# Kernel tuning notes

Measured on AMD Instinct MI355X. Metric: run time of the kernel, lower is better.

Reference implementation:

```python
import jax, jax.numpy as jnp
import numpy as np

THRESH = 0.5          # boundary_threshold
N_TARGET = 6.0        # target_avg_token_length
RATIO_W = 0.03        # ratio_loss_weight
LRD = 0.75            # learning_rate_difference
EPS = 1e-8            # torch cosine_similarity eps


def _frac_grad(t, frac):
    # value = t, gradient scaled by frac (straight-through)
    tg = t * frac
    return tg + jax.lax.stop_gradient(t - tg)


def _assoc_scan(gates, x):
    # h_t = gates_t * h_{t-1} + x_t, over axis 1. gates: [B,N], x: [B,N,D]
    def combine(a, b):
        ga, xa = a
        gb, xb = b
        return gb * ga, gb * xa + xb
    _, h = jax.lax.associative_scan(combine, (gates[..., None], x), axis=1)
    return h


def _forward(tokens, W_qk, start_key, W_res, b_res):
    B, L, D = tokens.shape
    # queries / keys projection
    qk = jnp.einsum('bld,de->ble', tokens, W_qk)
    q, k = jnp.split(qk, 2, axis=-1)
    # keys shifted right by one, start_key token prepended
    ks = jnp.concatenate([jnp.broadcast_to(start_key, (B, 1, k.shape[-1])), k[:, :-1]], axis=1)
    qn = jnp.linalg.norm(q, axis=-1)
    kn = jnp.linalg.norm(ks, axis=-1)
    cos = jnp.sum(q * ks, axis=-1) / jnp.maximum(qn * kn, EPS)
    probs = (1.0 - cos) * 0.5                              # [B,L]
    boundary = (probs > THRESH).at[:, 0].set(True)         # [B,L] bool
    num_chunks = boundary.sum(-1)                          # [B]
    chunk_id = jnp.cumsum(boundary.astype(jnp.int32), axis=1) - 1  # token -> chunk slot
    b_idx = jnp.broadcast_to(jnp.arange(B)[:, None], (B, L))
    slot = jnp.where(boundary, chunk_id, L)                # pad slot L for non-boundaries
    # padded (to worst-case L chunks) boundary tokens / probs — equals nested_tensor.to_padded_tensor
    down = jnp.zeros((B, L + 1, D), tokens.dtype).at[b_idx, slot].set(tokens)[:, :L]
    bprobs = jnp.zeros((B, L + 1), probs.dtype).at[b_idx, slot].set(probs)[:, :L]
    chunk_lens = jnp.zeros((B, L), jnp.int32).at[b_idx, chunk_id].add(1)  # tokens per chunk, 0-padded
    mask = jnp.arange(L)[None, :] < num_chunks[:, None]    # valid chunk slots
    gates = 1.0 - bprobs
    down = down * bprobs[..., None]
    confidence = jnp.where(boundary, probs, 1.0 - probs)
    scale = confidence + jax.lax.stop_gradient(1.0 - confidence)  # straight_through(confidence, 1.0)
    # aux ratio loss (straight-through fraction vectors)
    F_soft = jax.nn.sigmoid(probs - THRESH)
    F = (F_soft + jax.lax.stop_gradient(boundary.astype(probs.dtype) - F_soft)).mean(-1)
    G = probs.mean(-1)
    aux = (N_TARGET / (N_TARGET - 1.0)) * ((N_TARGET - 1.0) * F * G + (1.0 - F) * (1.0 - G))
    weighted_aux = aux.mean() * RATIO_W
    downsampled = _frac_grad(down, 1.0 / LRD)
    # ---- upsample(downsampled) ----
    scanned = _assoc_scan(gates, downsampled)              # smooth assoc scan over chunk slots
    # repeat_interleave by chunk_lens == gather chunk vector for each token position
    ups = jnp.take_along_axis(scanned, chunk_id[..., None], axis=1)  # [B,L,D]
    ups = ups * scale[..., None]
    ups = ups + jnp.einsum('bld,de->ble', tokens, W_res) + b_res     # residual_proj(residual)
    ups = _frac_grad(ups, LRD)
    return downsampled, ups, weighted_aux


def setup_inputs() -> dict:
    key = jax.random.key(0)
    k1, k2, k3, k4 = jax.random.split(key, 4)
    B, L, D, DQK = 8, 4096, 1024, 1024
    return {
        'tokens': jax.random.normal(k1, (B, L, D), jnp.float32),
        'W_qk': jax.random.normal(k2, (D, 2 * DQK), jnp.float32) * 0.02,
        'start_key': jax.random.normal(k3, (DQK,), jnp.float32) * 0.01,
        'W_res': jax.random.normal(k4, (D, D), jnp.float32) * 0.02,
        'b_res': jnp.zeros((D,), jnp.float32),
    }


def reference(tokens, W_qk, start_key, W_res, b_res):
    return _forward(tokens, W_qk, start_key, W_res, b_res)
```

## Files before the change

### kernel.cpp

```cpp
#include <hip/hip_runtime.h>
#include <hip/hip_fp16.h>
#include <cmath>

typedef unsigned short u16;
typedef _Float16 halfT;
typedef halfT v8h __attribute__((ext_vector_type(8)));
typedef float v4f __attribute__((ext_vector_type(4)));

#define B_   8
#define L_   4096
#define D_   1024
#define M_   32768
#define RCAP 8192

__global__ __launch_bounds__(256) void split_tok(const float* __restrict__ T,
    u16* __restrict__ Tf) {
  size_t id = (size_t)blockIdx.x * 256 + threadIdx.x;
  size_t base = id * 8;
  float4 v0 = *(const float4*)(T + base);
  float4 v1 = *(const float4*)(T + base + 4);
  float a[8] = {v0.x, v0.y, v0.z, v0.w, v1.x, v1.y, v1.z, v1.w};
  u16 h[8];
#pragma unroll
  for (int j = 0; j < 8; j++) h[j] = __half_as_ushort(__float2half(a[j]));
  *(uint4*)(Tf + base) = *(uint4*)h;
}

__global__ __launch_bounds__(256) void split_wT(const float* __restrict__ W,
    int N, u16* __restrict__ Wf) {
  int id = blockIdx.x * 256 + threadIdx.x;
  int n = id & (N - 1);
  int k0 = (id / N) * 8;
  u16 h[8];
#pragma unroll
  for (int j = 0; j < 8; j++)
    h[j] = __half_as_ushort(__float2half(W[(size_t)(k0 + j) * N + n]));
  *(uint4*)(Wf + (size_t)n * 1024 + k0) = *(uint4*)h;
}

__device__ __forceinline__ void gll16(const void* g, void* l) {
  __builtin_amdgcn_global_load_lds(
      (const __attribute__((address_space(1))) void*)g,
      (__attribute__((address_space(3))) void*)l, 16, 0, 0);
}

__global__ __launch_bounds__(256) void gemm_f16(
    const u16* __restrict__ Af, const u16* __restrict__ Bf,
    void* __restrict__ Cout, int N, int NTN, int mode,
    const float* __restrict__ Hs, const int* __restrict__ cid,
    const float* __restrict__ bres)
{
  __shared__ u16 ldsA[4096], ldsB[4096];
  const int tid = threadIdx.x;
  const int lane = tid & 63, w = tid >> 6;
  const int q = lane >> 4, fr = lane & 15;
  const int wr = w >> 1, wc = w & 1;
  int bid = blockIdx.x;
  int idx = bid >> 3, x = bid & 7;
  const int n0 = (idx % NTN) * 128;
  const int m0 = (x * 32 + idx / NTN) * 128;

  const u16* src = (w < 2) ? Af : Bf;
  const int rowbase = ((w < 2) ? m0 : n0) + (w & 1) * 64;
  u16* dst = ((w < 2) ? ldsA : ldsB) + (w & 1) * 2048;

  v4f acc[4][4];
#pragma unroll
  for (int i = 0; i < 4; i++)
#pragma unroll
    for (int j = 0; j < 4; j++) acc[i][j] = (v4f)0.f;

  for (int kt = 0; kt < 32; kt++) {
    const u16* sk = src + kt * 32;
#pragma unroll
    for (int j = 0; j < 4; j++) {
      int lam = j * 64 + lane;
      int mi = lam >> 2;
      int qq = (lam & 3) ^ ((lam >> 3) & 3);
      gll16(sk + (size_t)(rowbase + mi) * 1024 + qq * 8, dst + j * 512);
    }
    __syncthreads();
    v8h bh[4];
#pragma unroll
    for (int nt = 0; nt < 4; nt++) {
      int r = wc * 64 + nt * 16 + fr;
      int off = r * 32 + ((q ^ ((r >> 1) & 3)) << 3);
      bh[nt] = *(const v8h*)&ldsB[off];
    }
#pragma unroll
    for (int mt = 0; mt < 4; mt++) {
      int r = wr * 64 + mt * 16 + fr;
      int off = r * 32 + ((q ^ ((r >> 1) & 3)) << 3);
      v8h ah = *(const v8h*)&ldsA[off];
#pragma unroll
      for (int nt = 0; nt < 4; nt++)
        acc[mt][nt] = __builtin_amdgcn_mfma_f32_16x16x32_f16(ah, bh[nt], acc[mt][nt], 0, 0, 0);
    }
    __syncthreads();
  }

  if (mode == 0) {
    __half* C = (__half*)Cout;
#pragma unroll
    for (int mt = 0; mt < 4; mt++)
#pragma unroll
      for (int r = 0; r < 4; r++) {
        int grow = m0 + wr * 64 + mt * 16 + q * 4 + r;
        __half* crow = C + (size_t)grow * N + n0 + wc * 64 + fr;
#pragma unroll
        for (int nt = 0; nt < 4; nt++)
          crow[nt * 16] = __float2half(acc[mt][nt][r]);
      }
  } else {
    float* C = (float*)Cout;
#pragma unroll
    for (int mt = 0; mt < 4; mt++)
#pragma unroll
      for (int r = 0; r < 4; r++) {
        int grow = m0 + wr * 64 + mt * 16 + q * 4 + r;
        int b = grow >> 12;
        int cc = cid[grow];
        const float* hrow = Hs + (size_t)((b << 12) + cc) * 1024 + n0 + wc * 64 + fr;
        const float* brow = bres + n0 + wc * 64 + fr;
        float* crow = C + (size_t)grow * 1024 + n0 + wc * 64 + fr;
#pragma unroll
        for (int nt = 0; nt < 4; nt++)
          crow[nt * 16] = acc[mt][nt][r] + hrow[nt * 16] + brow[nt * 16];
      }
  }
}

__global__ __launch_bounds__(256) void probs_half(const __half* __restrict__ C1,
    const float* __restrict__ skey, float* __restrict__ probs)
{
  int gt = blockIdx.x * 256 + threadIdx.x;
  int wid = gt >> 6, lane = threadIdx.x & 63;
  float qv[16], kv[16];
  {
    const __half2* p2 = (const __half2*)(C1 + (size_t)wid * 2048 + lane * 16);
#pragma unroll
    for (int j = 0; j < 8; j++) {
      float2 f = __half22float2(p2[j]); qv[2 * j] = f.x; qv[2 * j + 1] = f.y;
    }
  }
  if ((wid & 4095) == 0) {
#pragma unroll
    for (int j = 0; j < 16; j++) kv[j] = skey[lane * 16 + j];
  } else {
    const __half2* p2 = (const __half2*)(C1 + (size_t)(wid - 1) * 2048 + 1024 + lane * 16);
#pragma unroll
    for (int j = 0; j < 8; j++) {
      float2 f = __half22float2(p2[j]); kv[2 * j] = f.x; kv[2 * j + 1] = f.y;
    }
  }
  float dq = 0.f, nq = 0.f, nk = 0.f;
#pragma unroll
  for (int j = 0; j < 16; j++) {
    dq += qv[j] * kv[j]; nq += qv[j] * qv[j]; nk += kv[j] * kv[j];
  }
#pragma unroll
  for (int off = 32; off > 0; off >>= 1) {
    dq += __shfl_down(dq, off);
    nq += __shfl_down(nq, off);
    nk += __shfl_down(nk, off);
  }
  if (lane == 0)
    probs[wid] = 0.5f * (1.f - dq / fmaxf(sqrtf(nq) * sqrtf(nk), 1e-8f));
}

__global__ void zero_cnt(int* __restrict__ cnt) {
  if (threadIdx.x == 0) *cnt = 0;
}

__global__ __launch_bounds__(256) void flag_kernel(
    const float* __restrict__ probs, int* __restrict__ flags,
    int* __restrict__ cnt)
{
  int gm = blockIdx.x * 256 + threadIdx.x;
  float cosv = 1.f - 2.f * probs[gm];
  if (fabsf(cosv) < 2.5e-4f) {
    int idx = atomicAdd(cnt, 1);
    if (idx < RCAP) flags[idx] = gm;
  }
}

__global__ __launch_bounds__(256) void recheck2(
    const float* __restrict__ tok, const float* __restrict__ Wqk,
    const float* __restrict__ sk, float* __restrict__ probs,
    const int* __restrict__ flags, const int* __restrict__ cnt)
{
  __shared__ float sq[1024], sp[1024];
  __shared__ double red[3][4];
  int nf = *cnt; if (nf > RCAP) nf = RCAP;
  int t = threadIdx.x;
  for (int fi = blockIdx.x; fi < nf; fi += gridDim.x) {
    int gm = flags[fi];
    int l = gm & 4095;
    const float* trow = tok + (size_t)gm * 1024;
    for (int j = t; j < 1024; j += 256) {
      sq[j] = trow[j];
      sp[j] = l ? trow[j - 1024] : 0.f;
    }
    __syncthreads();
    double qe0 = 0, qe1 = 0, qe2 = 0, qe3 = 0;
    double ke0 = 0, ke1 = 0, ke2 = 0, ke3 = 0;
    const float4* wq = (const float4*)Wqk + t;
    const float4* wk = (const float4*)(Wqk + 1024) + t;
#pragma unroll 4
    for (int d = 0; d < 1024; d++) {
      double td = (double)sq[d];
      double pd = (double)sp[d];
      float4 a = wq[(size_t)d * 512];
      float4 b = wk[(size_t)d * 512];
      qe0 += td * (double)a.x; qe1 += td * (double)a.y;
      qe2 += td * (double)a.z; qe3 += td * (double)a.w;
      ke0 += pd * (double)b.x; ke1 += pd * (double)b.y;
      ke2 += pd * (double)b.z; ke3 += pd * (double)b.w;
    }
    if (l == 0) {
      float4 s4 = *((const float4*)sk + t);
      ke0 = (double)s4.x; ke1 = (double)s4.y;
      ke2 = (double)s4.z; ke3 = (double)s4.w;
    }
    double dq = qe0 * ke0 + qe1 * ke1 + qe2 * ke2 + qe3 * ke3;
    double nq = qe0 * qe0 + qe1 * qe1 + qe2 * qe2 + qe3 * qe3;
    double nk = ke0 * ke0 + ke1 * ke1 + ke2 * ke2 + ke3 * ke3;
#pragma unroll
    for (int off = 32; off > 0; off >>= 1) {
      dq += __shfl_down(dq, off);
      nq += __shfl_down(nq, off);
      nk += __shfl_down(nk, off);
    }
    int w = t >> 6;
    if ((t & 63) == 0) { red[0][w] = dq; red[1][w] = nq; red[2][w] = nk; }
    __syncthreads();
    if (t == 0) {
      double DQ = red[0][0] + red[0][1] + red[0][2] + red[0][3];
      double NQ = red[1][0] + red[1][1] + red[1][2] + red[1][3];
      double NK = red[2][0] + red[2][1] + red[2][2] + red[2][3];
      double den = sqrt(NQ) * sqrt(NK);
      if (den < 1e-8) den = 1e-8;
      probs[gm] = (float)(0.5 * (1.0 - DQ / den));
    }
    __syncthreads();
  }
}

__global__ __launch_bounds__(256) void meta_kernel(
    const float* __restrict__ probs, int* __restrict__ cid,
    int* __restrict__ pos, float* __restrict__ cprob,
    int* __restrict__ numC, float* __restrict__ auxv)
{
  __shared__ int   sc[256];
  __shared__ float psh[256];
  int b = blockIdx.x, t = threadIdx.x;
  const float* pr = probs + b * 4096;
  int base = t * 16;
  float pv[16]; int loc[16]; bool bd[16];
  int cnt = 0; float ps = 0.f;
#pragma unroll
  for (int i = 0; i < 16; i++) {
    float p = pr[base + i];
    pv[i] = p; ps += p;
    bool bb = (base + i == 0) || (p > 0.5f);
    bd[i] = bb; cnt += bb ? 1 : 0; loc[i] = cnt;
  }
  sc[t] = cnt; psh[t] = ps;
  __syncthreads();
  for (int off = 1; off < 256; off <<= 1) {
    int add = (t >= off) ? sc[t - off] : 0;
    __syncthreads();
    sc[t] += add;
    __syncthreads();
  }
  int excl = sc[t] - cnt;
#pragma unroll
  for (int i = 0; i < 16; i++) {
    int c = excl + loc[i] - 1;
    cid[b * 4096 + base + i] = c;
    if (bd[i]) { pos[b * 4096 + c] = base + i; cprob[b * 4096 + c] = pv[i]; }
  }
  int total = sc[255];
  for (int off = 128; off > 0; off >>= 1) {
    if (t < off) psh[t] += psh[t + off];
    __syncthreads();
  }
  if (t == 0) {
    numC[b] = total;
    float F = (float)total / 4096.f;
    float G = psh[0] / 4096.f;
    auxv[b] = 1.2f * (5.f * F * G + (1.f - F) * (1.f - G));
  }
}

__global__ void aux_final(const float* __restrict__ auxv, float* __restrict__ out2)
{
  if (threadIdx.x == 0) {
    float s = 0.f;
    for (int i = 0; i < 8; i++) s += auxv[i];
    out2[0] = s * (0.03f / 8.f);
  }
}

__global__ __launch_bounds__(256) void down_kernel(
    const float* __restrict__ tok, const int* __restrict__ pos,
    const float* __restrict__ cprob, const int* __restrict__ numC,
    float* __restrict__ out0)
{
  int blk = blockIdx.x;
  int b = blk >> 12, slot = blk & 4095;
  float4 v = make_float4(0.f, 0.f, 0.f, 0.f);
  if (slot < numC[b]) {
    int l = pos[blk];
    float p = cprob[blk];
    float4 tv = *(const float4*)(tok + (size_t)((b << 12) + l) * 1024 + threadIdx.x * 4);
    v = make_float4(p * tv.x, p * tv.y, p * tv.z, p * tv.w);
  }
  *(float4*)(out0 + (size_t)blk * 1024 + threadIdx.x * 4) = v;
}

__global__ __launch_bounds__(256) void scanH_kernel(
    const float* __restrict__ out0, const float* __restrict__ cprob,
    const int* __restrict__ numC, float* __restrict__ H)
{
  int seg = blockIdx.x, b = blockIdx.y;
  int nc = numC[b];
  int cs = seg << 8;
  if (cs >= nc) return;
  int ce = min(cs + 256, nc);
  int c0 = (seg == 0) ? 0 : cs - 64;
  int off = threadIdx.x * 4;
  float hx = 0.f, hy = 0.f, hz = 0.f, hw = 0.f;
  int c = c0;
  for (; c < cs; c++) {
    float g = 1.f - cprob[(b << 12) + c];
    float4 xv = *(const float4*)(out0 + (size_t)((b << 12) + c) * 1024 + off);
    hx = fmaf(g, hx, xv.x); hy = fmaf(g, hy, xv.y);
    hz = fmaf(g, hz, xv.z); hw = fmaf(g, hw, xv.w);
  }
  for (; c < ce; c++) {
    float g = 1.f - cprob[(b << 12) + c];
    float4 xv = *(const float4*)(out0 + (size_t)((b << 12) + c) * 1024 + off);
    hx = fmaf(g, hx, xv.x); hy = fmaf(g, hy, xv.y);
    hz = fmaf(g, hz, xv.z); hw = fmaf(g, hw, xv.w);
    *(float4*)(H + (size_t)((b << 12) + c) * 1024 + off) = make_float4(hx, hy, hz, hw);
  }
}

extern "C" void kernel_launch(void* const* d_in, const int* in_sizes, int n_in,
                              void* d_out, int out_size, void* d_ws, size_t ws_size,
                              hipStream_t stream)
{
  const float* tokens = (const float*)d_in[0];
  const float* Wqk    = (const float*)d_in[1];
  const float* sk     = (const float*)d_in[2];
  const float* Wres   = (const float*)d_in[3];
  const float* bres   = (const float*)d_in[4];

  float* out0 = (float*)d_out;
  float* out1 = out0 + (size_t)M_ * D_;
  float* out2 = out1 + (size_t)M_ * D_;

  char* ws = (char*)d_ws;
  __half* C1h  = (__half*)ws;
  float*  Hbuf = (float*)ws;
  int*   rflags = (int*)ws;
  int*   rcnt   = (int*)(ws + (size_t)RCAP * 4);
  u16* Tf = (u16*)(ws + 134217728ull);
  u16* Wf = (u16*)(ws + 268435456ull);
  float* probs = (float*)(ws + 276824064ull);
  int*   cidp  = (int*)(ws + 276955136ull);
  int*   posp  = (int*)(ws + 277086208ull);
  float* cprob = (float*)(ws + 277217280ull);
  int*   numC  = (int*)(ws + 277348352ull);
  float* auxv  = (float*)(ws + 277348416ull);

  split_tok<<<16384, 256, 0, stream>>>(tokens, Tf);
  split_wT<<<1024, 256, 0, stream>>>(Wqk, 2048, Wf);
  gemm_f16<<<4096, 256, 0, stream>>>(Tf, Wf, C1h, 2048, 16, 0,
                                     nullptr, nullptr, nullptr);
  probs_half<<<8192, 256, 0, stream>>>(C1h, sk, probs);
  zero_cnt<<<1, 64, 0, stream>>>(rcnt);
  flag_kernel<<<128, 256, 0, stream>>>(probs, rflags, rcnt);
  recheck2<<<512, 256, 0, stream>>>(tokens, Wqk, sk, probs, rflags, rcnt);
  meta_kernel<<<8, 256, 0, stream>>>(probs, cidp, posp, cprob, numC, auxv);
  aux_final<<<1, 64, 0, stream>>>(auxv, out2);
  down_kernel<<<M_, 256, 0, stream>>>(tokens, posp, cprob, numC, out0);
  scanH_kernel<<<dim3(16, 8), 256, 0, stream>>>(out0, cprob, numC, Hbuf);
  split_wT<<<512, 256, 0, stream>>>(Wres, 1024, Wf);
  gemm_f16<<<2048, 256, 0, stream>>>(Tf, Wf, out1, 1024, 8, 1,
                                     Hbuf, cidp, bres);
}
```

Baseline: 992.1 us.

## Double GEMM K-tile, fuse flagging into probs kernel, vectorize half loads

The GEMM now stages a K=64 slice per iteration instead of K=32, using 8-wide XOR swizzling. This halves the loop iterations and barrier pairs, at the cost of twice the LDS footprint per block. The separate flag kernel is folded into probs_half, which now flags near-zero cosines with an atomic, and its half loads are widened to uint4. Recheck flags move into the out1 buffer, and the Wres transpose is hoisted into its own buffer early, removing one launch and reordering the small kernels.

```diff
diff --git a/kernel.cpp b/kernel.cpp
--- a/kernel.cpp
+++ b/kernel.cpp
@@ -50,7 +50,7 @@
     const float* __restrict__ Hs, const int* __restrict__ cid,
     const float* __restrict__ bres)
 {
-  __shared__ u16 ldsA[4096], ldsB[4096];
+  __shared__ u16 ldsA[8192], ldsB[8192];
   const int tid = threadIdx.x;
   const int lane = tid & 63, w = tid >> 6;
   const int q = lane >> 4, fr = lane & 15;
@@ -62,7 +62,10 @@
 
   const u16* src = (w < 2) ? Af : Bf;
   const int rowbase = ((w < 2) ? m0 : n0) + (w & 1) * 64;
-  u16* dst = ((w < 2) ? ldsA : ldsB) + (w & 1) * 2048;
+  u16* dst = ((w < 2) ? ldsA : ldsB) + (w & 1) * 4096;
+
+  const int lhi = lane >> 3;
+  const int swz = (lane & 7) ^ lhi;
 
   v4f acc[4][4];
 #pragma unroll
@@ -70,31 +73,34 @@
 #pragma unroll
     for (int j = 0; j < 4; j++) acc[i][j] = (v4f)0.f;
 
-  for (int kt = 0; kt < 32; kt++) {
-    const u16* sk = src + kt * 32;
-#pragma unroll
-    for (int j = 0; j < 4; j++) {
-      int lam = j * 64 + lane;
-      int mi = lam >> 2;
-      int qq = (lam & 3) ^ ((lam >> 3) & 3);
-      gll16(sk + (size_t)(rowbase + mi) * 1024 + qq * 8, dst + j * 512);
-    }
-    __syncthreads();
-    v8h bh[4];
+  for (int kt = 0; kt < 16; kt++) {
+    const u16* sk = src + kt * 64;
+#pragma unroll
+    for (int j = 0; j < 8; j++) {
+      int mi = j * 8 + lhi;
+      gll16(sk + (size_t)(rowbase + mi) * 1024 + swz * 8, dst + j * 512);
+    }
+    __syncthreads();
+    v8h bh[4][2];
 #pragma unroll
     for (int nt = 0; nt < 4; nt++) {
       int r = wc * 64 + nt * 16 + fr;
-      int off = r * 32 + ((q ^ ((r >> 1) & 3)) << 3);
-      bh[nt] = *(const v8h*)&ldsB[off];
+#pragma unroll
+      for (int kk = 0; kk < 2; kk++) {
+        int off = r * 64 + (((q + 4 * kk) ^ (r & 7)) << 3);
+        bh[nt][kk] = *(const v8h*)&ldsB[off];
+      }
     }
 #pragma unroll
     for (int mt = 0; mt < 4; mt++) {
       int r = wr * 64 + mt * 16 + fr;
-      int off = r * 32 + ((q ^ ((r >> 1) & 3)) << 3);
-      v8h ah = *(const v8h*)&ldsA[off];
-#pragma unroll
-      for (int nt = 0; nt < 4; nt++)
-        acc[mt][nt] = __builtin_amdgcn_mfma_f32_16x16x32_f16(ah, bh[nt], acc[mt][nt], 0, 0, 0);
+      v8h ah0 = *(const v8h*)&ldsA[r * 64 + ((q ^ (r & 7)) << 3)];
+      v8h ah1 = *(const v8h*)&ldsA[r * 64 + (((q + 4) ^ (r & 7)) << 3)];
+#pragma unroll
+      for (int nt = 0; nt < 4; nt++) {
+        acc[mt][nt] = __builtin_amdgcn_mfma_f32_16x16x32_f16(ah0, bh[nt][0], acc[mt][nt], 0, 0, 0);
+        acc[mt][nt] = __builtin_amdgcn_mfma_f32_16x16x32_f16(ah1, bh[nt][1], acc[mt][nt], 0, 0, 0);
+      }
     }
     __syncthreads();
   }
@@ -131,26 +137,33 @@
 }
 
 __global__ __launch_bounds__(256) void probs_half(const __half* __restrict__ C1,
-    const float* __restrict__ skey, float* __restrict__ probs)
+    const float* __restrict__ skey, float* __restrict__ probs,
+    int* __restrict__ flags, int* __restrict__ cnt)
 {
   int gt = blockIdx.x * 256 + threadIdx.x;
   int wid = gt >> 6, lane = threadIdx.x & 63;
   float qv[16], kv[16];
   {
-    const __half2* p2 = (const __half2*)(C1 + (size_t)wid * 2048 + lane * 16);
+    const uint4* p4 = (const uint4*)(C1 + (size_t)wid * 2048 + lane * 16);
+    uint4 u0 = p4[0], u1 = p4[1];
+    unsigned uu[8] = {u0.x, u0.y, u0.z, u0.w, u1.x, u1.y, u1.z, u1.w};
 #pragma unroll
     for (int j = 0; j < 8; j++) {
-      float2 f = __half22float2(p2[j]); qv[2 * j] = f.x; qv[2 * j + 1] = f.y;
+      float2 f = __half22float2(*(const __half2*)&uu[j]);
+      qv[2 * j] = f.x; qv[2 * j + 1] = f.y;
     }
   }
   if ((wid & 4095) == 0) {
 #pragma unroll
     for (int j = 0; j < 16; j++) kv[j] = skey[lane * 16 + j];
   } else {
-    const __half2* p2 = (const __half2*)(C1 + (size_t)(wid - 1) * 2048 + 1024 + lane * 16);
+    const uint4* p4 = (const uint4*)(C1 + (size_t)(wid - 1) * 2048 + 1024 + lane * 16);
+    uint4 u0 = p4[0], u1 = p4[1];
+    unsigned uu[8] = {u0.x, u0.y, u0.z, u0.w, u1.x, u1.y, u1.z, u1.w};
 #pragma unroll
     for (int j = 0; j < 8; j++) {
-      float2 f = __half22float2(p2[j]); kv[2 * j] = f.x; kv[2 * j + 1] = f.y;
+      float2 f = __half22float2(*(const __half2*)&uu[j]);
+      kv[2 * j] = f.x; kv[2 * j + 1] = f.y;
     }
   }
   float dq = 0.f, nq = 0.f, nk = 0.f;
@@ -164,24 +177,18 @@
     nq += __shfl_down(nq, off);
     nk += __shfl_down(nk, off);
   }
-  if (lane == 0)
-    probs[wid] = 0.5f * (1.f - dq / fmaxf(sqrtf(nq) * sqrtf(nk), 1e-8f));
+  if (lane == 0) {
+    float cosv = dq / fmaxf(sqrtf(nq) * sqrtf(nk), 1e-8f);
+    probs[wid] = 0.5f * (1.f - cosv);
+    if (fabsf(cosv) < 2.5e-4f) {
+      int idx = atomicAdd(cnt, 1);
+      if (idx < RCAP) flags[idx] = wid;
+    }
+  }
 }
 
 __global__ void zero_cnt(int* __restrict__ cnt) {
   if (threadIdx.x == 0) *cnt = 0;
-}
-
-__global__ __launch_bounds__(256) void flag_kernel(
-    const float* __restrict__ probs, int* __restrict__ flags,
-    int* __restrict__ cnt)
-{
-  int gm = blockIdx.x * 256 + threadIdx.x;
-  float cosv = 1.f - 2.f * probs[gm];
-  if (fabsf(cosv) < 2.5e-4f) {
-    int idx = atomicAdd(cnt, 1);
-    if (idx < RCAP) flags[idx] = gm;
-  }
 }
 
 __global__ __launch_bounds__(256) void recheck2(
@@ -364,30 +371,30 @@
   char* ws = (char*)d_ws;
   __half* C1h  = (__half*)ws;
   float*  Hbuf = (float*)ws;
-  int*   rflags = (int*)ws;
-  int*   rcnt   = (int*)(ws + (size_t)RCAP * 4);
-  u16* Tf = (u16*)(ws + 134217728ull);
-  u16* Wf = (u16*)(ws + 268435456ull);
+  u16* Tf  = (u16*)(ws + 134217728ull);
+  u16* Wf  = (u16*)(ws + 268435456ull);
+  u16* Wf2 = (u16*)(ws + 272629760ull);
   float* probs = (float*)(ws + 276824064ull);
   int*   cidp  = (int*)(ws + 276955136ull);
   int*   posp  = (int*)(ws + 277086208ull);
   float* cprob = (float*)(ws + 277217280ull);
   int*   numC  = (int*)(ws + 277348352ull);
   float* auxv  = (float*)(ws + 277348416ull);
+  int*   rflags = (int*)out1;
+  int*   rcnt   = rflags + RCAP;
 
   split_tok<<<16384, 256, 0, stream>>>(tokens, Tf);
   split_wT<<<1024, 256, 0, stream>>>(Wqk, 2048, Wf);
+  split_wT<<<512, 256, 0, stream>>>(Wres, 1024, Wf2);
+  zero_cnt<<<1, 64, 0, stream>>>(rcnt);
   gemm_f16<<<4096, 256, 0, stream>>>(Tf, Wf, C1h, 2048, 16, 0,
                                      nullptr, nullptr, nullptr);
-  probs_half<<<8192, 256, 0, stream>>>(C1h, sk, probs);
-  zero_cnt<<<1, 64, 0, stream>>>(rcnt);
-  flag_kernel<<<128, 256, 0, stream>>>(probs, rflags, rcnt);
+  probs_half<<<8192, 256, 0, stream>>>(C1h, sk, probs, rflags, rcnt);
   recheck2<<<512, 256, 0, stream>>>(tokens, Wqk, sk, probs, rflags, rcnt);
   meta_kernel<<<8, 256, 0, stream>>>(probs, cidp, posp, cprob, numC, auxv);
   aux_final<<<1, 64, 0, stream>>>(auxv, out2);
   down_kernel<<<M_, 256, 0, stream>>>(tokens, posp, cprob, numC, out0);
   scanH_kernel<<<dim3(16, 8), 256, 0, stream>>>(out0, cprob, numC, Hbuf);
-  split_wT<<<512, 256, 0, stream>>>(Wres, 1024, Wf);
-  gemm_f16<<<2048, 256, 0, stream>>>(Tf, Wf, out1, 1024, 8, 1,
+  gemm_f16<<<2048, 256, 0, stream>>>(Tf, Wf2, out1, 1024, 8, 1,
                                      Hbuf, cidp, bres);
 }
```

New measurement: 986.1 us. About the same (-0.6%).
